# Kernel tuning notes

Measured on AMD Instinct MI355X. Metric: run time of the kernel, lower is better.

The kernel has to match this reference:

```python
import jax, jax.numpy as jnp
import numpy as np

BLOCK = 64  # bnb NF4 blocksize

# NF4 quantile codebook (bitsandbytes quant_type='nf4')
NF4_CODEBOOK = jnp.array([
    -1.0, -0.6961928009986877, -0.5250730514526367, -0.39491748809814453,
    -0.28444138169288635, -0.18477343022823334, -0.09105003625154495, 0.0,
    0.07958029955625534, 0.16093020141124725, 0.24611230194568634,
    0.33791524171829224, 0.44070982933044434, 0.5626170039176941,
    0.7229568362236023, 1.0], dtype=jnp.float32)

IN_FEATURES = 4096
OUT_FEATURES = 11008


def setup_inputs() -> dict:
    key = jax.random.key(0)
    k1, k2, k3 = jax.random.split(key, 3)
    x = jax.random.normal(k1, (4, 2048, IN_FEATURES), dtype=jnp.float32)
    codes = jax.random.randint(k2, (OUT_FEATURES, IN_FEATURES), 0, 16, dtype=jnp.int32)
    n_blocks = OUT_FEATURES * IN_FEATURES // BLOCK
    absmax = jax.random.uniform(k3, (n_blocks,), dtype=jnp.float32)
    return {"x": x, "codes": codes, "absmax": absmax}


def dequant_nf4(codes, absmax):
    # codes: [out, in] int codes in [0,16); absmax: [out*in/BLOCK] per-block scale
    w = NF4_CODEBOOK[codes].reshape(-1, BLOCK)          # [n_blocks, BLOCK]
    w = w * absmax[:, None]                              # blockwise rescale
    return w.reshape(codes.shape)                        # [out, in]


def reference(x, codes, absmax):
    # y = x @ dequant(W)^T  (nn.Linear semantics, bias=False)
    W = dequant_nf4(codes, absmax)                       # [out, in]
    return jnp.einsum('bsi,oi->bso', x, W)
```

## Files before the change

### kernel.cpp

```cpp
#include <hip/hip_runtime.h>
#include <stdint.h>

typedef unsigned short u16;

#define IN_F   4096
#define OUT_F  11008
#define M_TOT  8192

__device__ __constant__ float NF4_TAB[16] = {
    -1.0f, -0.6961928009986877f, -0.5250730514526367f, -0.39491748809814453f,
    -0.28444138169288635f, -0.18477343022823334f, -0.09105003625154495f, 0.0f,
    0.07958029955625534f, 0.16093020141124725f, 0.24611230194568634f,
    0.33791524171829224f, 0.44070982933044434f, 0.5626170039176941f,
    0.7229568362236023f, 1.0f};

static __device__ __forceinline__ unsigned f2bf(float f) {
  unsigned u = __float_as_uint(f);
  u += 0x7fffu + ((u >> 16) & 1u);
  return u >> 16;
}

__global__ __launch_bounds__(256) void dequant_w_kernel(
    const int* __restrict__ codes, const float* __restrict__ absmax,
    uint4* __restrict__ wout, int n8) {
  __shared__ float lut[16];
  if (threadIdx.x < 16) lut[threadIdx.x] = NF4_TAB[threadIdx.x];
  __syncthreads();
  int t = blockIdx.x * 256 + threadIdx.x;
  if (t >= n8) return;
  const int4* cp = (const int4*)codes + (size_t)t * 2;
  int4 c0 = cp[0];
  int4 c1 = cp[1];
  float am = absmax[t >> 3];
  unsigned h0 = f2bf(lut[c0.x] * am) | (f2bf(lut[c0.y] * am) << 16);
  unsigned h1 = f2bf(lut[c0.z] * am) | (f2bf(lut[c0.w] * am) << 16);
  unsigned h2 = f2bf(lut[c1.x] * am) | (f2bf(lut[c1.y] * am) << 16);
  unsigned h3 = f2bf(lut[c1.z] * am) | (f2bf(lut[c1.w] * am) << 16);
  wout[t] = make_uint4(h0, h1, h2, h3);
}

__global__ __launch_bounds__(256) void convert_x_kernel(
    const float4* __restrict__ x, uint4* __restrict__ xout, int n8) {
  int t = blockIdx.x * 256 + threadIdx.x;
  if (t >= n8) return;
  float4 a = x[(size_t)t * 2];
  float4 b = x[(size_t)t * 2 + 1];
  unsigned h0 = f2bf(a.x) | (f2bf(a.y) << 16);
  unsigned h1 = f2bf(a.z) | (f2bf(a.w) << 16);
  unsigned h2 = f2bf(b.x) | (f2bf(b.y) << 16);
  unsigned h3 = f2bf(b.z) | (f2bf(b.w) << 16);
  xout[t] = make_uint4(h0, h1, h2, h3);
}

typedef __attribute__((ext_vector_type(8))) short short8;
typedef __attribute__((ext_vector_type(4))) float f32x4;

static __device__ __forceinline__ void async_copy16(const u16* g, u16* l) {
  __builtin_amdgcn_global_load_lds(
      (const __attribute__((address_space(1))) unsigned int*)g,
      (__attribute__((address_space(3))) unsigned int*)l, 16, 0, 0);
}

#define STAGE(BUF, KT)                                                       \
  do {                                                                       \
    async_copy16(agp + (size_t)(KT) * 32, &lds[BUF][wave * 512]);            \
    async_copy16(agp + (size_t)(KT) * 32 + (size_t)128 * IN_F,               \
                 &lds[BUF][4096 + wave * 512]);                              \
    async_copy16(bgp + (size_t)(KT) * 32, &lds[BUF][8192 + wave * 512]);     \
  } while (0)

#define KSTEP(BUF, TN)                                                       \
  do {                                                                       \
    short8 af[4], bf[4];                                                     \
    _Pragma("unroll") for (int i = 0; i < 4; ++i)                            \
        af[i] = *(const short8*)&lds[BUF][(wr * 64 + i * 16 + row16) * 32 +  \
                                          rsw];                              \
    _Pragma("unroll") for (int j = 0; j < 4; ++j)                            \
        bf[j] = *(const short8*)&lds[BUF][8192 +                             \
                                          (wc * 64 + j * 16 + row16) * 32 +  \
                                          rsw];                              \
    STAGE(BUF ^ 1, TN);                                                      \
    __builtin_amdgcn_s_setprio(1);                                           \
    _Pragma("unroll") for (int i = 0; i < 4; ++i)                            \
        _Pragma("unroll") for (int j = 0; j < 4; ++j)                        \
            acc[i][j] = __builtin_amdgcn_mfma_f32_16x16x32_bf16(             \
                af[i], bf[j], acc[i][j], 0, 0, 0);                           \
    __builtin_amdgcn_s_setprio(0);                                           \
    asm volatile("s_waitcnt vmcnt(0)\n\ts_barrier" ::: "memory");            \
  } while (0)

__global__ __launch_bounds__(512, 4) void gemm256x128_bt_bf16_kernel(
    const u16* __restrict__ A,
    const u16* __restrict__ B,
    float* __restrict__ C) {
  constexpr int K  = IN_F;
  constexpr int N  = OUT_F;
  constexpr int NT = K / 32;
  __shared__ u16 lds[2][(256 + 128) * 32];

  const int tid   = threadIdx.x;
  const int wave  = tid >> 6;
  const int lane  = tid & 63;
  const int wr    = wave >> 1;
  const int wc    = wave & 1;
  const int row16 = lane & 15;
  const int quad  = lane >> 4;
  const int rsw   = ((quad ^ (row16 & 3)) << 3);

  const int orig = blockIdx.x;
  const int tile = (orig & 7) * 344 + (orig >> 3);
  const int mb = tile / 86, nb = tile % 86;
  const int m0 = mb * 256, n0 = nb * 128;

  const int srow = lane >> 2;
  const int scol = ((lane & 3) ^ (srow & 3)) << 3;
  const u16* agp = A + (size_t)(m0 + wave * 16 + srow) * K + scol;
  const u16* bgp = B + (size_t)(n0 + wave * 16 + srow) * K + scol;

  f32x4 acc[4][4] = {};

  STAGE(0, 0);
  asm volatile("s_waitcnt vmcnt(0)\n\ts_barrier" ::: "memory");

  for (int t = 0; t < NT; t += 2) {
    const int t1 = t + 1;
    const int t2 = (t + 2 < NT) ? t + 2 : NT - 1;
    KSTEP(0, t1);
    KSTEP(1, t2);
  }

#pragma unroll
  for (int i = 0; i < 4; ++i)
#pragma unroll
    for (int j = 0; j < 4; ++j)
#pragma unroll
      for (int r = 0; r < 4; ++r)
        C[(size_t)(m0 + wr * 64 + i * 16 + quad * 4 + r) * N +
          (n0 + wc * 64 + j * 16 + row16)] = acc[i][j][r];
}

__global__ void fallback_kernel(const float* __restrict__ x,
                                const int* __restrict__ codes,
                                const float* __restrict__ absmax,
                                float* __restrict__ out) {
  __shared__ float lut[16];
  __shared__ float xs[16][17];
  __shared__ float ws[16][17];
  const int tx = threadIdx.x, ty = threadIdx.y;
  if (ty == 0 && tx < 16) lut[tx] = NF4_TAB[tx];
  __syncthreads();
  const int m  = blockIdx.y * 16 + ty;
  const int n0 = blockIdx.x * 16;
  float acc = 0.f;
  for (int k0 = 0; k0 < IN_F; k0 += 16) {
    xs[ty][tx] = x[(size_t)m * IN_F + k0 + tx];
    int idx = (n0 + ty) * IN_F + k0 + tx;
    ws[ty][tx] = lut[codes[idx]] * absmax[idx >> 6];
    __syncthreads();
#pragma unroll
    for (int kk = 0; kk < 16; ++kk) acc += xs[ty][kk] * ws[tx][kk];
    __syncthreads();
  }
  out[(size_t)m * OUT_F + n0 + tx] = acc;
}

extern "C" void kernel_launch(void* const* d_in, const int* in_sizes, int n_in,
                              void* d_out, int out_size, void* d_ws, size_t ws_size,
                              hipStream_t stream) {
  const float* x      = (const float*)d_in[0];
  const int*   codes  = (const int*)d_in[1];
  const float* absmax = (const float*)d_in[2];
  float* out = (float*)d_out;

  const size_t wBytes = (size_t)OUT_F * IN_F * 2;
  const size_t xBytes = (size_t)M_TOT * IN_F * 2;

  if (ws_size >= wBytes + xBytes) {
    u16* wq = (u16*)d_ws;
    u16* xq = (u16*)((char*)d_ws + wBytes);

    const int n8w = OUT_F * IN_F / 8;
    dequant_w_kernel<<<(n8w + 255) / 256, 256, 0, stream>>>(
        codes, absmax, (uint4*)wq, n8w);

    const int n8x = M_TOT * IN_F / 8;
    convert_x_kernel<<<(n8x + 255) / 256, 256, 0, stream>>>(
        (const float4*)x, (uint4*)xq, n8x);

    const int nwg = (M_TOT / 256) * (OUT_F / 128);
    gemm256x128_bt_bf16_kernel<<<nwg, 512, 0, stream>>>(xq, wq, out);
  } else {
    dim3 blk(16, 16);
    dim3 grid(OUT_F / 16, M_TOT / 16);
    fallback_kernel<<<grid, blk, 0, stream>>>(x, codes, absmax, out);
  }
}
```

Baseline: 1.244 ms.

## Triple-buffer LDS in GEMM with two-tile prefetch and new swizzle

Replaces the double-buffered LDS pipeline with a three-stage ring buffer. Two K-tiles are now in flight, and each iteration waits with vmcnt(3) instead of draining every load. The LDS XOR swizzle also changes to use (row>>1)&3, which is meant to cut bank conflicts on the short8 reads. LDS per block grows from 48KB to 72KB, which may lower occupancy below the 4 blocks-per-CU launch bound. Rotating the buffers through pointers may also add address arithmetic.

```diff
diff --git a/kernel.cpp b/kernel.cpp
--- a/kernel.cpp
+++ b/kernel.cpp
@@ -61,32 +61,12 @@
       (__attribute__((address_space(3))) unsigned int*)l, 16, 0, 0);
 }
 
-#define STAGE(BUF, KT)                                                       \
+#define STAGE(LP, KT)                                                        \
   do {                                                                       \
-    async_copy16(agp + (size_t)(KT) * 32, &lds[BUF][wave * 512]);            \
+    async_copy16(agp + (size_t)(KT) * 32, (LP) + wave * 512);                \
     async_copy16(agp + (size_t)(KT) * 32 + (size_t)128 * IN_F,               \
-                 &lds[BUF][4096 + wave * 512]);                              \
-    async_copy16(bgp + (size_t)(KT) * 32, &lds[BUF][8192 + wave * 512]);     \
-  } while (0)
-
-#define KSTEP(BUF, TN)                                                       \
-  do {                                                                       \
-    short8 af[4], bf[4];                                                     \
-    _Pragma("unroll") for (int i = 0; i < 4; ++i)                            \
-        af[i] = *(const short8*)&lds[BUF][(wr * 64 + i * 16 + row16) * 32 +  \
-                                          rsw];                              \
-    _Pragma("unroll") for (int j = 0; j < 4; ++j)                            \
-        bf[j] = *(const short8*)&lds[BUF][8192 +                             \
-                                          (wc * 64 + j * 16 + row16) * 32 +  \
-                                          rsw];                              \
-    STAGE(BUF ^ 1, TN);                                                      \
-    __builtin_amdgcn_s_setprio(1);                                           \
-    _Pragma("unroll") for (int i = 0; i < 4; ++i)                            \
-        _Pragma("unroll") for (int j = 0; j < 4; ++j)                        \
-            acc[i][j] = __builtin_amdgcn_mfma_f32_16x16x32_bf16(             \
-                af[i], bf[j], acc[i][j], 0, 0, 0);                           \
-    __builtin_amdgcn_s_setprio(0);                                           \
-    asm volatile("s_waitcnt vmcnt(0)\n\ts_barrier" ::: "memory");            \
+                 (LP) + 4096 + wave * 512);                                  \
+    async_copy16(bgp + (size_t)(KT) * 32, (LP) + 8192 + wave * 512);         \
   } while (0)
 
 __global__ __launch_bounds__(512, 4) void gemm256x128_bt_bf16_kernel(
@@ -96,7 +76,7 @@
   constexpr int K  = IN_F;
   constexpr int N  = OUT_F;
   constexpr int NT = K / 32;
-  __shared__ u16 lds[2][(256 + 128) * 32];
+  __shared__ u16 lds[3][(256 + 128) * 32];
 
   const int tid   = threadIdx.x;
   const int wave  = tid >> 6;
@@ -105,7 +85,7 @@
   const int wc    = wave & 1;
   const int row16 = lane & 15;
   const int quad  = lane >> 4;
-  const int rsw   = ((quad ^ (row16 & 3)) << 3);
+  const int rsw   = (quad ^ ((row16 >> 1) & 3)) << 3;
 
   const int orig = blockIdx.x;
   const int tile = (orig & 7) * 344 + (orig >> 3);
@@ -113,21 +93,42 @@
   const int m0 = mb * 256, n0 = nb * 128;
 
   const int srow = lane >> 2;
-  const int scol = ((lane & 3) ^ (srow & 3)) << 3;
+  const int scol = ((lane & 3) ^ ((lane >> 3) & 3)) << 3;
   const u16* agp = A + (size_t)(m0 + wave * 16 + srow) * K + scol;
   const u16* bgp = B + (size_t)(n0 + wave * 16 + srow) * K + scol;
 
   f32x4 acc[4][4] = {};
 
-  STAGE(0, 0);
-  asm volatile("s_waitcnt vmcnt(0)\n\ts_barrier" ::: "memory");
+  u16* s0 = &lds[0][0];
+  u16* s1 = &lds[1][0];
+  u16* s2 = &lds[2][0];
 
-  for (int t = 0; t < NT; t += 2) {
-    const int t1 = t + 1;
-    const int t2 = (t + 2 < NT) ? t + 2 : NT - 1;
-    KSTEP(0, t1);
-    KSTEP(1, t2);
+  STAGE(s0, 0);
+  STAGE(s1, 1);
+  asm volatile("s_waitcnt vmcnt(3)\n\ts_barrier" ::: "memory");
+
+  for (int t = 0; t < NT; ++t) {
+    const int tn = (t + 2 < NT) ? t + 2 : NT - 1;
+    STAGE(s2, tn);
+    short8 af[4], bf[4];
+#pragma unroll
+    for (int i = 0; i < 4; ++i)
+      af[i] = *(const short8*)&s0[(wr * 64 + i * 16 + row16) * 32 + rsw];
+#pragma unroll
+    for (int j = 0; j < 4; ++j)
+      bf[j] = *(const short8*)&s0[8192 + (wc * 64 + j * 16 + row16) * 32 + rsw];
+    __builtin_amdgcn_s_setprio(1);
+#pragma unroll
+    for (int i = 0; i < 4; ++i)
+#pragma unroll
+      for (int j = 0; j < 4; ++j)
+        acc[i][j] = __builtin_amdgcn_mfma_f32_16x16x32_bf16(
+            af[i], bf[j], acc[i][j], 0, 0, 0);
+    __builtin_amdgcn_s_setprio(0);
+    asm volatile("s_waitcnt vmcnt(3)\n\ts_barrier" ::: "memory");
+    u16* tmp = s0; s0 = s1; s1 = s2; s2 = tmp;
   }
+  asm volatile("s_waitcnt vmcnt(0)" ::: "memory");
 
 #pragma unroll
   for (int i = 0; i < 4; ++i)
```

Measured after the change: 1.215 ms. 1.02x faster.
